# Optimization experiments

Measured on AMD Instinct MI355X. Metric: run time of the kernel, lower is better.

## Reference

```python
import jax, jax.numpy as jnp
import numpy as np

BS, X_DIM, KEY_DIM, N_KEYS, TOPK = 16384, 4096, 512, 4096, 16


def setup_inputs() -> dict:
    key = jax.random.key(0)
    k_x, k_keys, k_w, k_b = jax.random.split(key, 4)
    bound = 1.0 / np.sqrt(X_DIM)  # torch Linear default init range
    return {
        "x": jax.random.normal(k_x, (BS, X_DIM), dtype=jnp.float32),
        "keys": jax.random.normal(k_keys, (N_KEYS, KEY_DIM), dtype=jnp.float32),
        "W": jax.random.uniform(k_w, (KEY_DIM, X_DIM), dtype=jnp.float32, minval=-bound, maxval=bound),
        "b": jax.random.uniform(k_b, (KEY_DIM,), dtype=jnp.float32, minval=-bound, maxval=bound),
        "topk": TOPK,
    }


def reference(x, keys, W, b, topk):
    # query = projection(x): [bs, key_dim]
    query = jnp.einsum("bx,kx->bk", x, W) + b
    # scores = query @ keys^T: [bs, n_keys]
    scores = jnp.einsum("bd,nd->bn", query, keys)
    real_topk = min(keys.shape[0], topk)
    topk_scores, topk_idx = jax.lax.top_k(scores, real_topk)  # [bs, k]
    bs = scores.shape[0]
    rows = jnp.arange(bs)[:, None]
    # scatter topk scores into a zero tensor, then softmax over the full row
    gates = jnp.zeros_like(scores).at[rows, topk_idx].set(topk_scores)
    gates = jax.nn.softmax(gates, axis=1)
    return (gates, scores)
```

## Files before the change

### kernel.cpp

```cpp
#include <hip/hip_runtime.h>
#include <stdint.h>

#define BS_T   16384
#define XDIM   4096
#define KDIM   512
#define NKEYS  4096
#define KTOP   16

typedef _Float16 half8  __attribute__((ext_vector_type(8)));
typedef float    floatx4 __attribute__((ext_vector_type(4)));

__device__ static inline void gload_lds16(const void* g, void* l) {
  __builtin_amdgcn_global_load_lds(
      (const __attribute__((address_space(1))) uint32_t*)(uintptr_t)g,
      (__attribute__((address_space(3))) uint32_t*)(uint32_t)(uintptr_t)l,
      16, 0, 0);
}

#define FULL_BAR() do { __builtin_amdgcn_sched_barrier(0); \
                        __builtin_amdgcn_s_barrier(); \
                        __builtin_amdgcn_sched_barrier(0); } while (0)

__global__ __launch_bounds__(256) void cvt_f32_f16_v(const float* __restrict__ in,
                                                     _Float16* __restrict__ out, int n8) {
  int stride = gridDim.x * 256;
  for (int i = blockIdx.x * 256 + threadIdx.x; i < n8; i += stride) {
    float4 v0 = ((const float4*)in)[2 * i];
    float4 v1 = ((const float4*)in)[2 * i + 1];
    half8 h = { (_Float16)v0.x, (_Float16)v0.y, (_Float16)v0.z, (_Float16)v0.w,
                (_Float16)v1.x, (_Float16)v1.y, (_Float16)v1.z, (_Float16)v1.w };
    ((half8*)out)[i] = h;
  }
}

__global__ __launch_bounds__(256, 2)
void gemm1_fused(const float* __restrict__ X, const _Float16* __restrict__ Wh,
                 const float* __restrict__ bias, _Float16* __restrict__ Q) {
  __shared__ __align__(16) _Float16 ldsA[2][64 * 64];
  __shared__ __align__(16) _Float16 ldsB[2][256 * 64];

  const int tid  = threadIdx.x;
  const int lane = tid & 63;
  const int wid  = tid >> 6;
  const int cpx  = gridDim.x >> 3;
  const int bid  = (blockIdx.x & 7) * cpx + (blockIdx.x >> 3);
  const int rowBase = (bid >> 1) * 64;
  const int colBase = (bid & 1) * 256;
  const int wc  = wid * 64;
  const int l15 = lane & 15;
  const int q4  = lane >> 4;
  const int sub   = lane >> 3;
  const int gslot = (lane & 7) ^ sub;

  const int arow  = tid >> 3;
  const int aslot = tid & 7;
  const float* aSrc0 = X + (size_t)(rowBase + arow) * XDIM + aslot * 8;
  const float* aSrc1 = aSrc0 + (size_t)32 * XDIM;
  const int aoff = arow * 128 + ((aslot * 16) ^ ((arow & 7) << 4));
  char* const aD0 = (char*)&ldsA[0][0] + aoff;
  char* const aD1 = (char*)&ldsA[1][0] + aoff;
  const _Float16* const bSrc = Wh + (size_t)(colBase + wc + sub) * XDIM + gslot * 8;
  char* const bD0 = (char*)&ldsB[0][0] + wid * 8192;
  char* const bD1 = (char*)&ldsB[1][0] + wid * 8192;

  floatx4 acc[4][4];
  #pragma unroll
  for (int m = 0; m < 4; ++m)
    #pragma unroll
    for (int n = 0; n < 4; ++n)
      acc[m][n] = (floatx4)0.0f;

  auto stageB = [&](int kt, char* bd) {
    #pragma unroll
    for (int i = 0; i < 8; ++i)
      gload_lds16(bSrc + (size_t)i * 8 * XDIM + kt, bd + i * 1024);
  };
  auto writeA = [&](char* ad, float4 v00, float4 v01, float4 v10, float4 v11) {
    half8 h0 = { (_Float16)v00.x, (_Float16)v00.y, (_Float16)v00.z, (_Float16)v00.w,
                 (_Float16)v01.x, (_Float16)v01.y, (_Float16)v01.z, (_Float16)v01.w };
    half8 h1 = { (_Float16)v10.x, (_Float16)v10.y, (_Float16)v10.z, (_Float16)v10.w,
                 (_Float16)v11.x, (_Float16)v11.y, (_Float16)v11.z, (_Float16)v11.w };
    *(half8*)ad = h0;
    *(half8*)(ad + 4096) = h1;
  };
  auto compute = [&](const char* bA, const char* bB) {
    #pragma unroll
    for (int ks = 0; ks < 2; ++ks) {
      const int s = ks * 4 + q4;
      half8 a[4], b[4];
      #pragma unroll
      for (int m = 0; m < 4; ++m) {
        int row = m * 16 + l15;
        a[m] = *(const half8*)(bA + row * 128 + ((s * 16) ^ ((row & 7) << 4)));
      }
      #pragma unroll
      for (int n = 0; n < 4; ++n) {
        int row = wc + n * 16 + l15;
        b[n] = *(const half8*)(bB + row * 128 + ((s * 16) ^ ((row & 7) << 4)));
      }
      #pragma unroll
      for (int m = 0; m < 4; ++m)
        #pragma unroll
        for (int n = 0; n < 4; ++n)
          acc[m][n] = __builtin_amdgcn_mfma_f32_16x16x32_f16(a[m], b[n], acc[m][n], 0, 0, 0);
    }
  };

  {
    float4 v00 = *(const float4*)(aSrc0);
    float4 v01 = *(const float4*)(aSrc0 + 4);
    float4 v10 = *(const float4*)(aSrc1);
    float4 v11 = *(const float4*)(aSrc1 + 4);
    stageB(0, bD0);
    writeA(aD0, v00, v01, v10, v11);
  }
  __syncthreads();

  #pragma unroll 2
  for (int t = 0; t < 64; ++t) {
    const int pc = t & 1;
    const char* bA = pc ? (const char*)&ldsA[1][0] : (const char*)&ldsA[0][0];
    const char* bB = pc ? (const char*)&ldsB[1][0] : (const char*)&ldsB[0][0];
    char* adN = pc ? aD0 : aD1;
    char* bdN = pc ? bD0 : bD1;

    float4 v00, v01, v10, v11;
    if (t < 63) {
      const int ktn = (t + 1) * 64;
      v00 = *(const float4*)(aSrc0 + ktn);
      v01 = *(const float4*)(aSrc0 + ktn + 4);
      v10 = *(const float4*)(aSrc1 + ktn);
      v11 = *(const float4*)(aSrc1 + ktn + 4);
      stageB(ktn, bdN);
    }
    compute(bA, bB);
    if (t < 63) writeA(adN, v00, v01, v10, v11);
    __syncthreads();
  }

  #pragma unroll
  for (int m = 0; m < 4; ++m) {
    #pragma unroll
    for (int n = 0; n < 4; ++n) {
      int col = colBase + wc + n * 16 + l15;
      float bv = bias[col];
      #pragma unroll
      for (int r = 0; r < 4; ++r) {
        int row = rowBase + m * 16 + q4 * 4 + r;
        Q[(size_t)row * KDIM + col] = (_Float16)(acc[m][n][r] + bv);
      }
    }
  }
}

__global__ __launch_bounds__(512, 2)
void gemm2_pipe(const _Float16* __restrict__ Aq, const _Float16* __restrict__ Bk,
                float* __restrict__ outp) {
  __shared__ __align__(16) _Float16 ldsA[2][256 * 64];
  __shared__ __align__(16) _Float16 ldsB[2][256 * 64];

  const int tid  = threadIdx.x;
  const int lane = tid & 63;
  const int wid  = tid >> 6;
  const int cpx  = gridDim.x >> 3;
  const int bid  = (blockIdx.x & 7) * cpx + (blockIdx.x >> 3);
  const int nCol = NKEYS / 256;
  const int rowBase = (bid / nCol) * 256;
  const int colBase = (bid % nCol) * 256;
  const int wm = wid >> 2;
  const int wn = wid & 3;
  const int l15 = lane & 15;
  const int q4  = lane >> 4;
  const int sub   = lane >> 3;
  const int gslot = (lane & 7) ^ sub;

  const _Float16* aSrc = Aq + (size_t)rowBase * KDIM;
  const _Float16* bSrc = Bk + (size_t)colBase * KDIM;

  auto stageHalf = [&](const _Float16* src, char* ldsbase, int kt, int h) {
    #pragma unroll
    for (int j = 0; j < 2; ++j) {
      int g = h * 16 + wid * 2 + j;
      gload_lds16(src + (size_t)(g * 8 + sub) * KDIM + kt + gslot * 8,
                  ldsbase + g * 1024);
    }
  };
  auto ld8 = [&](const char* base, int row, int s) {
    return *(const half8*)(base + row * 128 + ((s * 16) ^ ((row & 7) << 4)));
  };

  floatx4 acc[8][4];
  #pragma unroll
  for (int m = 0; m < 8; ++m)
    #pragma unroll
    for (int n = 0; n < 4; ++n)
      acc[m][n] = (floatx4)0.0f;

  stageHalf(aSrc, (char*)ldsA[0], 0, 0);
  stageHalf(aSrc, (char*)ldsA[0], 0, 1);
  stageHalf(bSrc, (char*)ldsB[0], 0, 0);
  stageHalf(bSrc, (char*)ldsB[0], 0, 1);
  stageHalf(aSrc, (char*)ldsA[1], 64, 0);
  stageHalf(aSrc, (char*)ldsA[1], 64, 1);
  stageHalf(bSrc, (char*)ldsB[1], 64, 0);
  stageHalf(bSrc, (char*)ldsB[1], 64, 1);
  asm volatile("s_waitcnt vmcnt(8)" ::: "memory");
  FULL_BAR();

  for (int t = 0; t < 8; ++t) {
    const char* bA = (const char*)ldsA[t & 1];
    const char* bB = (const char*)ldsB[t & 1];
    char* sA = (char*)ldsA[t & 1];
    char* sB = (char*)ldsB[t & 1];
    const int ktn = (t + 2) * 64;
    const bool st = (t < 6);

    half8 a[4][2], b[4][2];

    #pragma unroll
    for (int m = 0; m < 4; ++m)
      #pragma unroll
      for (int kk = 0; kk < 2; ++kk)
        a[m][kk] = ld8(bA, wm * 128 + m * 16 + l15, kk * 4 + q4);
    #pragma unroll
    for (int n = 0; n < 4; ++n)
      #pragma unroll
      for (int kk = 0; kk < 2; ++kk)
        b[n][kk] = ld8(bB, wn * 64 + n * 16 + l15, kk * 4 + q4);
    FULL_BAR();
    asm volatile("s_waitcnt lgkmcnt(0)" ::: "memory");
    __builtin_amdgcn_sched_barrier(0);
    __builtin_amdgcn_s_setprio(1);
    #pragma unroll
    for (int m = 0; m < 4; ++m)
      #pragma unroll
      for (int n = 0; n < 2; ++n)
        #pragma unroll
        for (int kk = 0; kk < 2; ++kk)
          acc[m][n] = __builtin_amdgcn_mfma_f32_16x16x32_f16(a[m][kk], b[n][kk], acc[m][n], 0, 0, 0);
    __builtin_amdgcn_s_setprio(0);
    FULL_BAR();

    if (st) stageHalf(bSrc, sB, ktn, 0);
    __builtin_amdgcn_sched_barrier(0);
    __builtin_amdgcn_s_setprio(1);
    #pragma unroll
    for (int m = 0; m < 4; ++m)
      #pragma unroll
      for (int n = 2; n < 4; ++n)
        #pragma unroll
        for (int kk = 0; kk < 2; ++kk)
          acc[m][n] = __builtin_amdgcn_mfma_f32_16x16x32_f16(a[m][kk], b[n][kk], acc[m][n], 0, 0, 0);
    __builtin_amdgcn_s_setprio(0);
    FULL_BAR();

    #pragma unroll
    for (int m = 0; m < 4; ++m)
      #pragma unroll
      for (int kk = 0; kk < 2; ++kk)
        a[m][kk] = ld8(bA, wm * 128 + (m + 4) * 16 + l15, kk * 4 + q4);
    if (st) stageHalf(bSrc, sB, ktn, 1);
    FULL_BAR();
    asm volatile("s_waitcnt lgkmcnt(0)" ::: "memory");
    __builtin_amdgcn_sched_barrier(0);
    __builtin_amdgcn_s_setprio(1);
    #pragma unroll
    for (int m = 0; m < 4; ++m)
      #pragma unroll
      for (int n = 0; n < 2; ++n)
        #pragma unroll
        for (int kk = 0; kk < 2; ++kk)
          acc[m + 4][n] = __builtin_amdgcn_mfma_f32_16x16x32_f16(a[m][kk], b[n][kk], acc[m + 4][n], 0, 0, 0);
    __builtin_amdgcn_s_setprio(0);
    FULL_BAR();

    if (st) { stageHalf(aSrc, sA, ktn, 0); stageHalf(aSrc, sA, ktn, 1); }
    __builtin_amdgcn_sched_barrier(0);
    __builtin_amdgcn_s_setprio(1);
    #pragma unroll
    for (int m = 0; m < 4; ++m)
      #pragma unroll
      for (int n = 2; n < 4; ++n)
        #pragma unroll
        for (int kk = 0; kk < 2; ++kk)
          acc[m + 4][n] = __builtin_amdgcn_mfma_f32_16x16x32_f16(a[m][kk], b[n][kk], acc[m + 4][n], 0, 0, 0);
    __builtin_amdgcn_s_setprio(0);
    __builtin_amdgcn_sched_barrier(0);
    if (t < 6)      asm volatile("s_waitcnt vmcnt(8)" ::: "memory");
    else if (t == 6) asm volatile("s_waitcnt vmcnt(0)" ::: "memory");
    FULL_BAR();
  }

  #pragma unroll
  for (int m = 0; m < 8; ++m) {
    #pragma unroll
    for (int n = 0; n < 4; ++n) {
      int col = colBase + wn * 64 + n * 16 + l15;
      #pragma unroll
      for (int r = 0; r < 4; ++r) {
        int row = rowBase + wm * 128 + m * 16 + q4 * 4 + r;
        outp[(size_t)row * NKEYS + col] = acc[m][n][r];
      }
    }
  }
}

__global__ __launch_bounds__(256) void topk_gates_kernel(const float* __restrict__ scores,
                                                         float* __restrict__ gates) {
  __shared__ uint32_t hist[4096];
  __shared__ uint32_t sA[256];
  __shared__ uint32_t av[16], ai[16];
  __shared__ uint32_t sk[KTOP], si[KTOP];
  __shared__ uint32_t cntA, cntC;
  __shared__ int s_p; __shared__ uint32_t s_above;
  __shared__ float gk[KTOP]; __shared__ float s_gother;

  const int tid  = threadIdx.x;
  const int lane = tid & 63;
  const int w    = tid >> 6;
  const float* srow = scores + (size_t)blockIdx.x * NKEYS;

  uint4 z4 = {0, 0, 0, 0};
  #pragma unroll
  for (int i = 0; i < 4; ++i) ((uint4*)hist)[tid + 256 * i] = z4;
  if (tid == 0) { cntA = 0; cntC = 0; }

  uint32_t key[16];
  const int base = (w << 10) + (lane << 4);
  {
    const float4* p4 = (const float4*)(srow + base);
    #pragma unroll
    for (int i = 0; i < 4; ++i) {
      float4 t = p4[i];
      float tv[4] = { t.x, t.y, t.z, t.w };
      #pragma unroll
      for (int c = 0; c < 4; ++c) {
        uint32_t u = __float_as_uint(tv[c]);
        key[i * 4 + c] = u ^ (uint32_t)(((int32_t)u >> 31) | 0x80000000);
      }
    }
  }
  __syncthreads();

  #pragma unroll
  for (int j = 0; j < 16; ++j) atomicAdd(&hist[key[j] >> 20], 1u);
  __syncthreads();

  uint32_t h[16];
  #pragma unroll
  for (int i = 0; i < 16; ++i) h[i] = hist[tid * 16 + i];
  uint32_t sfx[17]; sfx[16] = 0;
  #pragma unroll
  for (int i = 15; i >= 0; --i) sfx[i] = sfx[i + 1] + h[i];
  sA[tid] = sfx[0];
  __syncthreads();
  uint32_t s = sfx[0];
  #pragma unroll
  for (int off = 1; off < 256; off <<= 1) {
    uint32_t add = (tid + off < 256) ? sA[tid + off] : 0;
    __syncthreads();
    s += add; sA[tid] = s;
    __syncthreads();
  }
  const uint32_t exclHi = s - sfx[0];

  #pragma unroll
  for (int i = 0; i < 16; ++i) {
    uint32_t cg = exclHi + sfx[i + 1];
    if (cg < KTOP && cg + h[i] >= KTOP) { s_p = tid * 16 + i; s_above = cg; }
  }
  __syncthreads();
  const uint32_t p = (uint32_t)s_p;
  const uint32_t above = s_above;
  const uint32_t need = KTOP - above;

  uint32_t* ck = hist;
  uint32_t* ci = hist + 2048;
  #pragma unroll
  for (int j = 0; j < 16; ++j) {
    uint32_t b = key[j] >> 20;
    if (b >= p) {
      uint32_t idx = (uint32_t)(base + j);
      if (b > p) { uint32_t pos = atomicAdd(&cntA, 1u); av[pos] = key[j]; ai[pos] = idx; }
      else       { uint32_t pos = atomicAdd(&cntC, 1u); if (pos < 2048u) { ck[pos] = key[j]; ci[pos] = idx; } }
    }
  }
  __syncthreads();

  const uint32_t nA = cntA;
  if (tid < nA) { sk[tid] = av[tid]; si[tid] = ai[tid]; }

  if (w == 0) {
    const uint32_t nC = min(cntC, 2048u);
    for (uint32_t k = 0; k < need; ++k) {
      uint32_t bk = 0, bi = 0xFFFFFFFFu, bp = 0;
      for (uint32_t c = lane; c < nC; c += 64) {
        uint32_t kk = ck[c], ii = ci[c];
        if (kk > bk || (kk == bk && ii < bi)) { bk = kk; bi = ii; bp = c; }
      }
      #pragma unroll
      for (int off = 32; off >= 1; off >>= 1) {
        uint32_t ok = __shfl_down(bk, off);
        uint32_t oi = __shfl_down(bi, off);
        uint32_t op = __shfl_down(bp, off);
        if (ok > bk || (ok == bk && oi < bi)) { bk = ok; bi = oi; bp = op; }
      }
      bp = __shfl(bp, 0);
      if (lane == 0) { ck[bp] = 0; sk[nA + k] = bk; si[nA + k] = bi; }
    }
  }
  __syncthreads();

  if (tid == 0) {
    float f[KTOP]; float mx = 0.f;
    #pragma unroll
    for (int k = 0; k < KTOP; ++k) {
      uint32_t kk = sk[k];
      float fv = (kk & 0x80000000u) ? __uint_as_float(kk ^ 0x80000000u)
                                    : __uint_as_float(~kk);
      f[k] = fv; mx = fmaxf(mx, fv);
    }
    float eo = __expf(-mx);
    float Z = (float)(NKEYS - KTOP) * eo;
    float e[KTOP];
    #pragma unroll
    for (int k = 0; k < KTOP; ++k) { e[k] = __expf(f[k] - mx); Z += e[k]; }
    float inv = 1.f / Z;
    #pragma unroll
    for (int k = 0; k < KTOP; ++k) gk[k] = e[k] * inv;
    s_gother = eo * inv;
  }
  __syncthreads();

  float go = s_gother;
  float4 g4 = { go, go, go, go };
  float* grow = gates + (size_t)blockIdx.x * NKEYS;
  #pragma unroll
  for (int j = 0; j < 4; ++j) ((float4*)grow)[j * 256 + tid] = g4;
  __syncthreads();
  if (tid < KTOP) grow[si[tid]] = gk[tid];
}

extern "C" void kernel_launch(void* const* d_in, const int* in_sizes, int n_in,
                              void* d_out, int out_size, void* d_ws, size_t ws_size,
                              hipStream_t stream) {
  const float* x    = (const float*)d_in[0];
  const float* keys = (const float*)d_in[1];
  const float* W    = (const float*)d_in[2];
  const float* bias = (const float*)d_in[3];
  (void)in_sizes; (void)n_in; (void)out_size; (void)ws_size;

  float* gates  = (float*)d_out;
  float* scores = (float*)d_out + (size_t)BS_T * NKEYS;

  _Float16* W_h = (_Float16*)d_ws;
  _Float16* k_h = W_h + (size_t)KDIM * XDIM;
  _Float16* q_h = k_h + (size_t)NKEYS * KDIM;

  cvt_f32_f16_v<<<dim3(1024), dim3(256), 0, stream>>>(W, W_h, KDIM * XDIM / 8);
  cvt_f32_f16_v<<<dim3(1024), dim3(256), 0, stream>>>(keys, k_h, NKEYS * KDIM / 8);

  gemm1_fused<<<dim3((BS_T / 64) * 2), dim3(256), 0, stream>>>(x, W_h, bias, q_h);

  gemm2_pipe<<<dim3((BS_T / 256) * (NKEYS / 256)), dim3(512), 0, stream>>>(
      q_h, k_h, scores);

  topk_gates_kernel<<<dim3(BS_T), dim3(256), 0, stream>>>(scores, gates);
}
```

Baseline: 359.9 us.

## Restructure gemm1 into 512-thread full-width tiles with split-phase pipelined MFMA

Result: faster. 351.8 us (-2.3%).

```diff
diff --git a/kernel.cpp b/kernel.cpp
--- a/kernel.cpp
+++ b/kernel.cpp
@@ -33,19 +33,16 @@
   }
 }
 
-__global__ __launch_bounds__(256, 2)
-void gemm1_fused(const float* __restrict__ X, const _Float16* __restrict__ Wh,
-                 const float* __restrict__ bias, _Float16* __restrict__ Q) {
+__global__ __launch_bounds__(512, 1)
+void gemm1_pipe(const float* __restrict__ X, const _Float16* __restrict__ Wh,
+                const float* __restrict__ bias, _Float16* __restrict__ Q) {
   __shared__ __align__(16) _Float16 ldsA[2][64 * 64];
-  __shared__ __align__(16) _Float16 ldsB[2][256 * 64];
+  __shared__ __align__(16) _Float16 ldsB[2][512 * 64];
 
   const int tid  = threadIdx.x;
   const int lane = tid & 63;
   const int wid  = tid >> 6;
-  const int cpx  = gridDim.x >> 3;
-  const int bid  = (blockIdx.x & 7) * cpx + (blockIdx.x >> 3);
-  const int rowBase = (bid >> 1) * 64;
-  const int colBase = (bid & 1) * 256;
+  const int rowBase = blockIdx.x * 64;
   const int wc  = wid * 64;
   const int l15 = lane & 15;
   const int q4  = lane >> 4;
@@ -54,95 +51,105 @@
 
   const int arow  = tid >> 3;
   const int aslot = tid & 7;
-  const float* aSrc0 = X + (size_t)(rowBase + arow) * XDIM + aslot * 8;
-  const float* aSrc1 = aSrc0 + (size_t)32 * XDIM;
+  const float* aSrcT = X + (size_t)(rowBase + arow) * XDIM + aslot * 8;
   const int aoff = arow * 128 + ((aslot * 16) ^ ((arow & 7) << 4));
-  char* const aD0 = (char*)&ldsA[0][0] + aoff;
-  char* const aD1 = (char*)&ldsA[1][0] + aoff;
-  const _Float16* const bSrc = Wh + (size_t)(colBase + wc + sub) * XDIM + gslot * 8;
-  char* const bD0 = (char*)&ldsB[0][0] + wid * 8192;
-  char* const bD1 = (char*)&ldsB[1][0] + wid * 8192;
-
-  floatx4 acc[4][4];
-  #pragma unroll
-  for (int m = 0; m < 4; ++m)
-    #pragma unroll
-    for (int n = 0; n < 4; ++n)
-      acc[m][n] = (floatx4)0.0f;
-
-  auto stageB = [&](int kt, char* bd) {
+  const _Float16* const bSrc = Wh + (size_t)(wc + sub) * XDIM + gslot * 8;
+
+  auto stageB = [&](int kt, int buf) {
+    char* bd = (char*)&ldsB[buf][0] + wid * 8192;
     #pragma unroll
     for (int i = 0; i < 8; ++i)
       gload_lds16(bSrc + (size_t)i * 8 * XDIM + kt, bd + i * 1024);
   };
-  auto writeA = [&](char* ad, float4 v00, float4 v01, float4 v10, float4 v11) {
-    half8 h0 = { (_Float16)v00.x, (_Float16)v00.y, (_Float16)v00.z, (_Float16)v00.w,
-                 (_Float16)v01.x, (_Float16)v01.y, (_Float16)v01.z, (_Float16)v01.w };
-    half8 h1 = { (_Float16)v10.x, (_Float16)v10.y, (_Float16)v10.z, (_Float16)v10.w,
-                 (_Float16)v11.x, (_Float16)v11.y, (_Float16)v11.z, (_Float16)v11.w };
-    *(half8*)ad = h0;
-    *(half8*)(ad + 4096) = h1;
+  auto writeA = [&](int buf, float4 v0, float4 v1) {
+    half8 h = { (_Float16)v0.x, (_Float16)v0.y, (_Float16)v0.z, (_Float16)v0.w,
+                (_Float16)v1.x, (_Float16)v1.y, (_Float16)v1.z, (_Float16)v1.w };
+    *(half8*)((char*)&ldsA[buf][0] + aoff) = h;
   };
-  auto compute = [&](const char* bA, const char* bB) {
-    #pragma unroll
-    for (int ks = 0; ks < 2; ++ks) {
-      const int s = ks * 4 + q4;
-      half8 a[4], b[4];
-      #pragma unroll
-      for (int m = 0; m < 4; ++m) {
-        int row = m * 16 + l15;
-        a[m] = *(const half8*)(bA + row * 128 + ((s * 16) ^ ((row & 7) << 4)));
-      }
-      #pragma unroll
-      for (int n = 0; n < 4; ++n) {
-        int row = wc + n * 16 + l15;
-        b[n] = *(const half8*)(bB + row * 128 + ((s * 16) ^ ((row & 7) << 4)));
-      }
-      #pragma unroll
-      for (int m = 0; m < 4; ++m)
-        #pragma unroll
-        for (int n = 0; n < 4; ++n)
-          acc[m][n] = __builtin_amdgcn_mfma_f32_16x16x32_f16(a[m], b[n], acc[m][n], 0, 0, 0);
-    }
+  auto ld8 = [&](const char* base, int row, int s) {
+    return *(const half8*)(base + row * 128 + ((s * 16) ^ ((row & 7) << 4)));
   };
 
-  {
-    float4 v00 = *(const float4*)(aSrc0);
-    float4 v01 = *(const float4*)(aSrc0 + 4);
-    float4 v10 = *(const float4*)(aSrc1);
-    float4 v11 = *(const float4*)(aSrc1 + 4);
-    stageB(0, bD0);
-    writeA(aD0, v00, v01, v10, v11);
-  }
-  __syncthreads();
-
-  #pragma unroll 2
+  floatx4 acc[4][4];
+  #pragma unroll
+  for (int m = 0; m < 4; ++m)
+    #pragma unroll
+    for (int n = 0; n < 4; ++n)
+      acc[m][n] = (floatx4)0.0f;
+
+  float4 p00 = *(const float4*)(aSrcT);
+  float4 p01 = *(const float4*)(aSrcT + 4);
+  float4 aw0 = *(const float4*)(aSrcT + 64);
+  float4 aw1 = *(const float4*)(aSrcT + 68);
+  stageB(0, 0);
+  stageB(64, 1);
+  writeA(0, p00, p01);
+  asm volatile("s_waitcnt vmcnt(8)" ::: "memory");
+  asm volatile("s_waitcnt lgkmcnt(0)" ::: "memory");
+  __builtin_amdgcn_sched_barrier(0);
+  __builtin_amdgcn_s_barrier();
+  __builtin_amdgcn_sched_barrier(0);
+
   for (int t = 0; t < 64; ++t) {
-    const int pc = t & 1;
-    const char* bA = pc ? (const char*)&ldsA[1][0] : (const char*)&ldsA[0][0];
-    const char* bB = pc ? (const char*)&ldsB[1][0] : (const char*)&ldsB[0][0];
-    char* adN = pc ? aD0 : aD1;
-    char* bdN = pc ? bD0 : bD1;
-
-    float4 v00, v01, v10, v11;
-    if (t < 63) {
-      const int ktn = (t + 1) * 64;
-      v00 = *(const float4*)(aSrc0 + ktn);
-      v01 = *(const float4*)(aSrc0 + ktn + 4);
-      v10 = *(const float4*)(aSrc1 + ktn);
-      v11 = *(const float4*)(aSrc1 + ktn + 4);
-      stageB(ktn, bdN);
-    }
-    compute(bA, bB);
-    if (t < 63) writeA(adN, v00, v01, v10, v11);
-    __syncthreads();
+    const int cu = t & 1;
+    const char* bA = (const char*)&ldsA[cu][0];
+    const char* bB = (const char*)&ldsB[cu][0];
+    half8 a[4][2], b[4][2];
+
+    #pragma unroll
+    for (int m = 0; m < 4; ++m)
+      #pragma unroll
+      for (int kk = 0; kk < 2; ++kk)
+        a[m][kk] = ld8(bA, m * 16 + l15, kk * 4 + q4);
+    #pragma unroll
+    for (int n = 0; n < 4; ++n)
+      #pragma unroll
+      for (int kk = 0; kk < 2; ++kk)
+        b[n][kk] = ld8(bB, wc + n * 16 + l15, kk * 4 + q4);
+    float4 nl0, nl1;
+    if (t < 62) {
+      nl0 = *(const float4*)(aSrcT + (t + 2) * 64);
+      nl1 = *(const float4*)(aSrcT + (t + 2) * 64 + 4);
+    }
+    FULL_BAR();
+    asm volatile("s_waitcnt lgkmcnt(0)" ::: "memory");
+    __builtin_amdgcn_sched_barrier(0);
+    __builtin_amdgcn_s_setprio(1);
+    #pragma unroll
+    for (int m = 0; m < 4; ++m)
+      #pragma unroll
+      for (int n = 0; n < 2; ++n)
+        #pragma unroll
+        for (int kk = 0; kk < 2; ++kk)
+          acc[m][n] = __builtin_amdgcn_mfma_f32_16x16x32_f16(a[m][kk], b[n][kk], acc[m][n], 0, 0, 0);
+    __builtin_amdgcn_s_setprio(0);
+    FULL_BAR();
+
+    if (t < 62) stageB((t + 2) * 64, cu);
+    if (t < 63) writeA(cu ^ 1, aw0, aw1);
+    asm volatile("s_waitcnt lgkmcnt(0)" ::: "memory");
+    __builtin_amdgcn_sched_barrier(0);
+    __builtin_amdgcn_s_setprio(1);
+    #pragma unroll
+    for (int m = 0; m < 4; ++m)
+      #pragma unroll
+      for (int n = 2; n < 4; ++n)
+        #pragma unroll
+        for (int kk = 0; kk < 2; ++kk)
+          acc[m][n] = __builtin_amdgcn_mfma_f32_16x16x32_f16(a[m][kk], b[n][kk], acc[m][n], 0, 0, 0);
+    __builtin_amdgcn_s_setprio(0);
+    __builtin_amdgcn_sched_barrier(0);
+    if (t < 62)       asm volatile("s_waitcnt vmcnt(10)" ::: "memory");
+    else if (t == 62) asm volatile("s_waitcnt vmcnt(0)"  ::: "memory");
+    FULL_BAR();
+    aw0 = nl0; aw1 = nl1;
   }
 
   #pragma unroll
   for (int m = 0; m < 4; ++m) {
     #pragma unroll
     for (int n = 0; n < 4; ++n) {
-      int col = colBase + wc + n * 16 + l15;
+      int col = wc + n * 16 + l15;
       float bv = bias[col];
       #pragma unroll
       for (int r = 0; r < 4; ++r) {
@@ -460,7 +467,7 @@
   cvt_f32_f16_v<<<dim3(1024), dim3(256), 0, stream>>>(W, W_h, KDIM * XDIM / 8);
   cvt_f32_f16_v<<<dim3(1024), dim3(256), 0, stream>>>(keys, k_h, NKEYS * KDIM / 8);
 
-  gemm1_fused<<<dim3((BS_T / 64) * 2), dim3(256), 0, stream>>>(x, W_h, bias, q_h);
+  gemm1_pipe<<<dim3(BS_T / 64), dim3(512), 0, stream>>>(x, W_h, bias, q_h);
 
   gemm2_pipe<<<dim3((BS_T / 256) * (NKEYS / 256)), dim3(512), 0, stream>>>(
       q_h, k_h, scores);
```

## Widen gemm1 tile to full 512 output columns per block

Applied to the files above, without the earlier changes.

New measurement: 357.8 us. Within noise of the previous version (-0.6%).

```diff
diff --git a/kernel.cpp b/kernel.cpp
--- a/kernel.cpp
+++ b/kernel.cpp
@@ -33,19 +33,16 @@
   }
 }
 
-__global__ __launch_bounds__(256, 2)
+__global__ __launch_bounds__(512, 2)
 void gemm1_fused(const float* __restrict__ X, const _Float16* __restrict__ Wh,
                  const float* __restrict__ bias, _Float16* __restrict__ Q) {
   __shared__ __align__(16) _Float16 ldsA[2][64 * 64];
-  __shared__ __align__(16) _Float16 ldsB[2][256 * 64];
+  __shared__ __align__(16) _Float16 ldsB[2][512 * 64];
 
   const int tid  = threadIdx.x;
   const int lane = tid & 63;
   const int wid  = tid >> 6;
-  const int cpx  = gridDim.x >> 3;
-  const int bid  = (blockIdx.x & 7) * cpx + (blockIdx.x >> 3);
-  const int rowBase = (bid >> 1) * 64;
-  const int colBase = (bid & 1) * 256;
+  const int rowBase = blockIdx.x * 64;
   const int wc  = wid * 64;
   const int l15 = lane & 15;
   const int q4  = lane >> 4;
@@ -54,14 +51,10 @@
 
   const int arow  = tid >> 3;
   const int aslot = tid & 7;
-  const float* aSrc0 = X + (size_t)(rowBase + arow) * XDIM + aslot * 8;
-  const float* aSrc1 = aSrc0 + (size_t)32 * XDIM;
-  const int aoff = arow * 128 + ((aslot * 16) ^ ((arow & 7) << 4));
-  char* const aD0 = (char*)&ldsA[0][0] + aoff;
-  char* const aD1 = (char*)&ldsA[1][0] + aoff;
-  const _Float16* const bSrc = Wh + (size_t)(colBase + wc + sub) * XDIM + gslot * 8;
-  char* const bD0 = (char*)&ldsB[0][0] + wid * 8192;
-  char* const bD1 = (char*)&ldsB[1][0] + wid * 8192;
+  const float* aSrc = X + (size_t)(rowBase + arow) * XDIM + aslot * 8;
+  char* aDst[2];
+  aDst[0] = (char*)&ldsA[0][0] + arow * 128 + ((aslot * 16) ^ ((arow & 7) << 4));
+  aDst[1] = (char*)&ldsA[1][0] + arow * 128 + ((aslot * 16) ^ ((arow & 7) << 4));
 
   floatx4 acc[4][4];
   #pragma unroll
@@ -70,20 +63,22 @@
     for (int n = 0; n < 4; ++n)
       acc[m][n] = (floatx4)0.0f;
 
-  auto stageB = [&](int kt, char* bd) {
-    #pragma unroll
-    for (int i = 0; i < 8; ++i)
-      gload_lds16(bSrc + (size_t)i * 8 * XDIM + kt, bd + i * 1024);
+  auto stageB = [&](int kt, int buf) {
+    #pragma unroll
+    for (int i = 0; i < 8; ++i) {
+      int g = wid * 8 + i;
+      gload_lds16(Wh + (size_t)(g * 8 + sub) * XDIM + kt + gslot * 8,
+                  (char*)&ldsB[buf][0] + g * 1024);
+    }
   };
-  auto writeA = [&](char* ad, float4 v00, float4 v01, float4 v10, float4 v11) {
-    half8 h0 = { (_Float16)v00.x, (_Float16)v00.y, (_Float16)v00.z, (_Float16)v00.w,
-                 (_Float16)v01.x, (_Float16)v01.y, (_Float16)v01.z, (_Float16)v01.w };
-    half8 h1 = { (_Float16)v10.x, (_Float16)v10.y, (_Float16)v10.z, (_Float16)v10.w,
-                 (_Float16)v11.x, (_Float16)v11.y, (_Float16)v11.z, (_Float16)v11.w };
-    *(half8*)ad = h0;
-    *(half8*)(ad + 4096) = h1;
+  auto writeA = [&](float4 v0, float4 v1, int buf) {
+    half8 h = { (_Float16)v0.x, (_Float16)v0.y, (_Float16)v0.z, (_Float16)v0.w,
+                (_Float16)v1.x, (_Float16)v1.y, (_Float16)v1.z, (_Float16)v1.w };
+    *(half8*)aDst[buf] = h;
   };
-  auto compute = [&](const char* bA, const char* bB) {
+  auto compute = [&](int buf) {
+    const char* bA = (const char*)&ldsA[buf][0];
+    const char* bB = (const char*)&ldsB[buf][0];
     #pragma unroll
     for (int ks = 0; ks < 2; ++ks) {
       const int s = ks * 4 + q4;
@@ -107,42 +102,32 @@
   };
 
   {
-    float4 v00 = *(const float4*)(aSrc0);
-    float4 v01 = *(const float4*)(aSrc0 + 4);
-    float4 v10 = *(const float4*)(aSrc1);
-    float4 v11 = *(const float4*)(aSrc1 + 4);
-    stageB(0, bD0);
-    writeA(aD0, v00, v01, v10, v11);
-  }
-  __syncthreads();
-
+    float4 v0 = *(const float4*)(aSrc + 0);
+    float4 v1 = *(const float4*)(aSrc + 4);
+    stageB(0, 0);
+    writeA(v0, v1, 0);
+  }
+  __syncthreads();
+
+  int cur = 0;
   #pragma unroll 2
-  for (int t = 0; t < 64; ++t) {
-    const int pc = t & 1;
-    const char* bA = pc ? (const char*)&ldsA[1][0] : (const char*)&ldsA[0][0];
-    const char* bB = pc ? (const char*)&ldsB[1][0] : (const char*)&ldsB[0][0];
-    char* adN = pc ? aD0 : aD1;
-    char* bdN = pc ? bD0 : bD1;
-
-    float4 v00, v01, v10, v11;
-    if (t < 63) {
-      const int ktn = (t + 1) * 64;
-      v00 = *(const float4*)(aSrc0 + ktn);
-      v01 = *(const float4*)(aSrc0 + ktn + 4);
-      v10 = *(const float4*)(aSrc1 + ktn);
-      v11 = *(const float4*)(aSrc1 + ktn + 4);
-      stageB(ktn, bdN);
-    }
-    compute(bA, bB);
-    if (t < 63) writeA(adN, v00, v01, v10, v11);
+  for (int t = 0; t < 63; ++t) {
+    const int ktn = (t + 1) * 64;
+    float4 v0 = *(const float4*)(aSrc + ktn);
+    float4 v1 = *(const float4*)(aSrc + ktn + 4);
+    stageB(ktn, cur ^ 1);
+    compute(cur);
+    writeA(v0, v1, cur ^ 1);
     __syncthreads();
-  }
+    cur ^= 1;
+  }
+  compute(cur);
 
   #pragma unroll
   for (int m = 0; m < 4; ++m) {
     #pragma unroll
     for (int n = 0; n < 4; ++n) {
-      int col = colBase + wc + n * 16 + l15;
+      int col = wc + n * 16 + l15;
       float bv = bias[col];
       #pragma unroll
       for (int r = 0; r < 4; ++r) {
@@ -460,7 +445,7 @@
   cvt_f32_f16_v<<<dim3(1024), dim3(256), 0, stream>>>(W, W_h, KDIM * XDIM / 8);
   cvt_f32_f16_v<<<dim3(1024), dim3(256), 0, stream>>>(keys, k_h, NKEYS * KDIM / 8);
 
-  gemm1_fused<<<dim3((BS_T / 64) * 2), dim3(256), 0, stream>>>(x, W_h, bias, q_h);
+  gemm1_fused<<<dim3(BS_T / 64), dim3(512), 0, stream>>>(x, W_h, bias, q_h);
 
   gemm2_pipe<<<dim3((BS_T / 256) * (NKEYS / 256)), dim3(512), 0, stream>>>(
       q_h, k_h, scores);
```
